# Optimization experiments

Measured on AMD Instinct MI355X. Metric: run time of the kernel, lower is better.

The kernel has to match this reference:

```python
import jax, jax.numpy as jnp
import numpy as np

L, D, H, R = 8, 1024, 16, 16
HD = D // H  # head dim


def setup_inputs() -> dict:
    key = jax.random.key(0)
    ks = jax.random.split(key, 7)
    s = 0.02  # init scale for stability
    return {
        "x": jax.random.normal(ks[0], (2, 1024, D), jnp.float32),
        "Wqkv": jax.random.normal(ks[1], (L, D, 3 * D), jnp.float32) * s,
        "Aqkv": jax.random.normal(ks[2], (L, D, R), jnp.float32) * s,
        "Bqkv": jax.random.normal(ks[3], (L, R, 3 * D), jnp.float32) * s,
        "Wproj": jax.random.normal(ks[4], (L, D, D), jnp.float32) * s,
        "Aproj": jax.random.normal(ks[5], (L, D, R), jnp.float32) * s,
        "Bproj": jax.random.normal(ks[6], (L, R, D), jnp.float32) * s,
    }


def _forward(x, Wqkv, Aqkv, Bqkv, Wproj, Aproj, Bproj):
    B, S, _ = x.shape
    # causal mask [S, S]
    mask = jnp.tril(jnp.ones((S, S), bool))

    def layer(h, p):
        Wq, Aq, Bq, Wp, Ap, Bp = p
        # LoRA merge exactly as the module: p + A @ B, then dense matmul
        Wq_m = Wq + Aq @ Bq            # [D, 3D]
        Wp_m = Wp + Ap @ Bp            # [D, D]
        qkv = h @ Wq_m                 # [B, S, 3D]
        q, k, v = jnp.split(qkv, 3, axis=-1)
        q = q.reshape(B, S, H, HD).transpose(0, 2, 1, 3)  # [B,H,S,hd]
        k = k.reshape(B, S, H, HD).transpose(0, 2, 1, 3)
        v = v.reshape(B, S, H, HD).transpose(0, 2, 1, 3)
        scores = jnp.einsum("bhqd,bhkd->bhqk", q, k) / np.sqrt(HD)
        scores = jnp.where(mask, scores, jnp.finfo(scores.dtype).min)
        attn = jax.nn.softmax(scores, axis=-1)
        o = jnp.einsum("bhqk,bhkd->bhqd", attn, v)        # [B,H,S,hd]
        o = o.transpose(0, 2, 1, 3).reshape(B, S, D)
        return h + o @ Wp_m, None

    out, _ = jax.lax.scan(layer, x, (Wqkv, Aqkv, Bqkv, Wproj, Aproj, Bproj))
    return out


def reference(x, Wqkv, Aqkv, Bqkv, Wproj, Aproj, Bproj):
    return _forward(x, Wqkv, Aqkv, Bqkv, Wproj, Aproj, Bproj)
```

## Files before the change

### kernel.cpp

```cpp
#include <hip/hip_runtime.h>
#include <hip/hip_bf16.h>


typedef unsigned short ushort_t;
typedef __attribute__((ext_vector_type(8))) short bf16x8;
typedef __attribute__((ext_vector_type(4))) float f32x4;

__device__ __forceinline__ unsigned short f2bf(float f) {
    union { float f; unsigned int u; } x; x.f = f;
    unsigned int r = x.u + 0x7fffu + ((x.u >> 16) & 1u);
    return (unsigned short)(r >> 16);
}

__device__ __forceinline__ f32x4 mfma16(bf16x8 a, bf16x8 b, f32x4 c) {
    return __builtin_amdgcn_mfma_f32_16x16x32_bf16(a, b, c, 0, 0, 0);
}

typedef const __attribute__((address_space(1))) unsigned int* gas_ptr;
typedef __attribute__((address_space(3))) unsigned int* las_ptr;
__device__ __forceinline__ void lds_stage16(const void* g, void* l) {
    __builtin_amdgcn_global_load_lds((gas_ptr)(unsigned long long)g,
                                     (las_ptr)(unsigned int)(unsigned long long)l,
                                     16, 0, 0);
}

#define RORMAX(x, C)                                                           \
    x = fmaxf(x, __int_as_float(__builtin_amdgcn_mov_dpp(                      \
                     __float_as_int(x), C, 0xf, 0xf, false)));
#define RORADD(x, C)                                                           \
    x += __int_as_float(__builtin_amdgcn_mov_dpp(                              \
        __float_as_int(x), C, 0xf, 0xf, false));

__global__ __launch_bounds__(256) void convert_x(
    const float4* __restrict__ in, float4* __restrict__ outF,
    ushort4* __restrict__ outB, int n4) {
    int i = blockIdx.x * 256 + threadIdx.x;
    if (i < n4) {
        float4 v = in[i];
        outF[i] = v;
        ushort4 o;
        o.x = f2bf(v.x); o.y = f2bf(v.y); o.z = f2bf(v.z); o.w = f2bf(v.w);
        outB[i] = o;
    }
}

__global__ __launch_bounds__(256) void merge_T2(
    const float* __restrict__ Wq, const float* __restrict__ Aq,
    const float* __restrict__ Bq, unsigned short* __restrict__ WTq,
    const float* __restrict__ Wp, const float* __restrict__ Ap,
    const float* __restrict__ Bp, unsigned short* __restrict__ WTp) {
    __shared__ float t[32][132];
    __shared__ float Asl[32][17];
    int bid = blockIdx.x;
    const float *W, *A, *Bm;
    unsigned short* WT;
    int N, bx, by, bz;
    if (bid < 6144) {
        N = 3072; bx = bid % 24; int u = bid / 24; by = u & 31; bz = u >> 5;
        W = Wq; A = Aq; Bm = Bq; WT = WTq;
    } else {
        bid -= 6144;
        N = 1024; bx = bid & 7; int u = bid >> 3; by = u & 31; bz = u >> 5;
        W = Wp; A = Ap; Bm = Bp; WT = WTp;
    }
    W  += (size_t)bz * 1024 * N;
    A  += (size_t)bz * 1024 * 16;
    Bm += (size_t)bz * 16 * N;
    WT += (size_t)bz * N * 1024;
    int j0 = bx * 128, i0 = by * 32;
    int tx = threadIdx.x & 31, ty = threadIdx.x >> 5;

    if (threadIdx.x < 128) {
        int r = threadIdx.x >> 2, c4 = (threadIdx.x & 3) * 4;
        float4 a = *(const float4*)&A[(size_t)(i0 + r) * 16 + c4];
        Asl[r][c4 + 0] = a.x; Asl[r][c4 + 1] = a.y;
        Asl[r][c4 + 2] = a.z; Asl[r][c4 + 3] = a.w;
    }
    float4 bv[16];
    #pragma unroll
    for (int r = 0; r < 16; r++)
        bv[r] = *(const float4*)&Bm[(size_t)r * N + j0 + tx * 4];
    float4 wv[4];
    #pragma unroll
    for (int ii0 = 0; ii0 < 4; ii0++)
        wv[ii0] = *(const float4*)&W[(size_t)(i0 + ty + ii0 * 8) * N + j0 + tx * 4];
    __builtin_amdgcn_sched_barrier(0);
    __syncthreads();

    #pragma unroll
    for (int ii0 = 0; ii0 < 4; ii0++) {
        int ii = ty + ii0 * 8;
        float4 acc = wv[ii0];
        #pragma unroll
        for (int r = 0; r < 16; r++) {
            float a = Asl[ii][r];
            acc.x += a * bv[r].x; acc.y += a * bv[r].y;
            acc.z += a * bv[r].z; acc.w += a * bv[r].w;
        }
        *(float4*)&t[ii][tx * 4] = acc;
    }
    __syncthreads();
    int jj = threadIdx.x >> 1, half = threadIdx.x & 1;
    bf16x8 o0, o1;
    #pragma unroll
    for (int c = 0; c < 8; c++) o0[c] = (short)f2bf(t[half * 16 + c][jj]);
    #pragma unroll
    for (int c = 0; c < 8; c++) o1[c] = (short)f2bf(t[half * 16 + 8 + c][jj]);
    unsigned short* dst = &WT[(size_t)(j0 + jj) * 1024 + i0 + half * 16];
    *(bf16x8*)dst = o0;
    *(bf16x8*)(dst + 8) = o1;
}

__global__ __launch_bounds__(256) void gemm_bf16_128(
    const unsigned short* __restrict__ A,
    const unsigned short* __restrict__ BT,
    unsigned short* __restrict__ outB,
    unsigned short* __restrict__ VT,
    int M, int N, int K) {
    __shared__ __align__(16) unsigned short As[2][128 * 32];
    __shared__ __align__(16) unsigned short Bs[2][128 * 32];
    const int tid = threadIdx.x;
    const int m0 = blockIdx.y * 128, n0 = blockIdx.x * 128;
    const int w = tid >> 6, lane = tid & 63;
    const int wm = (w >> 1) * 64, wn = (w & 1) * 64;
    const int lr = lane & 15, quad = lane >> 4;
    const int srow = w * 16 + (lane >> 2);
    const int skof = (lane & 3) * 8;

    f32x4 acc[4][4] = {};

    for (int k0 = 0; k0 < K; k0 += 64) {
        __syncthreads();
        #pragma unroll
        for (int h = 0; h < 2; h++) {
            lds_stage16(A  + (size_t)(m0 + srow)      * K + k0 + h * 32 + skof,
                        (char*)As[h] + w * 1024);
            lds_stage16(A  + (size_t)(m0 + 64 + srow) * K + k0 + h * 32 + skof,
                        (char*)As[h] + 4096 + w * 1024);
            lds_stage16(BT + (size_t)(n0 + srow)      * K + k0 + h * 32 + skof,
                        (char*)Bs[h] + w * 1024);
            lds_stage16(BT + (size_t)(n0 + 64 + srow) * K + k0 + h * 32 + skof,
                        (char*)Bs[h] + 4096 + w * 1024);
        }
        __syncthreads();

        #pragma unroll
        for (int h = 0; h < 2; h++) {
            bf16x8 af[4], bfr[4];
            #pragma unroll
            for (int i = 0; i < 4; i++) {
                af[i]  = *(const bf16x8*)&As[h][(wm + i * 16 + lr) * 32 + quad * 8];
                bfr[i] = *(const bf16x8*)&Bs[h][(wn + i * 16 + lr) * 32 + quad * 8];
            }
            #pragma unroll
            for (int i = 0; i < 4; i++)
                #pragma unroll
                for (int j = 0; j < 4; j++)
                    acc[i][j] = mfma16(af[i], bfr[j], acc[i][j]);
        }
    }
    if (n0 < 2048) {
        #pragma unroll
        for (int i = 0; i < 4; i++)
            #pragma unroll
            for (int j = 0; j < 4; j++)
                #pragma unroll
                for (int r = 0; r < 4; r++) {
                    int row = m0 + wm + i * 16 + quad * 4 + r;
                    int col = n0 + wn + j * 16 + lr;
                    float v = acc[i][j][r];
                    if (col < 1024) v *= 0.125f;
                    outB[(size_t)row * N + col] = f2bf(v);
                }
    } else {
        const int b = m0 >> 10;
        #pragma unroll
        for (int i = 0; i < 4; i++) {
            int row0 = m0 + wm + i * 16 + quad * 4;
            int s = row0 & 1023;
            #pragma unroll
            for (int j = 0; j < 4; j++) {
                int hd = n0 - 2048 + wn + j * 16 + lr;
                ushort4 o;
                o.x = f2bf(acc[i][j][0]); o.y = f2bf(acc[i][j][1]);
                o.z = f2bf(acc[i][j][2]); o.w = f2bf(acc[i][j][3]);
                *(ushort4*)&VT[((size_t)b * 1024 + hd) * 1024 + s] = o;
            }
        }
    }
}

__global__ __launch_bounds__(256) void gemm_bf16_64(
    const unsigned short* __restrict__ A,
    const unsigned short* __restrict__ BT,
    const float* __restrict__ res,
    float* __restrict__ outF,
    unsigned short* __restrict__ outB,
    int M, int N, int K) {
    __shared__ __align__(16) unsigned short As[2][2][64 * 32];
    __shared__ __align__(16) unsigned short Bs[2][2][64 * 32];
    const int tid = threadIdx.x;
    const int m0 = blockIdx.y * 64, n0 = blockIdx.x * 64;
    const int w = tid >> 6, lane = tid & 63;
    const int wm = (w >> 1) * 32, wn = (w & 1) * 32;
    const int lr = lane & 15, quad = lane >> 4;
    const int srow = w * 16 + (lane >> 2);
    const int skof = (lane & 3) * 8;

    f32x4 acc[2][2] = {};

    auto stage = [&](int k0, int buf) {
        #pragma unroll
        for (int h = 0; h < 2; h++) {
            lds_stage16(A  + (size_t)(m0 + srow) * K + k0 + h * 32 + skof,
                        (char*)As[buf][h] + w * 1024);
            lds_stage16(BT + (size_t)(n0 + srow) * K + k0 + h * 32 + skof,
                        (char*)Bs[buf][h] + w * 1024);
        }
    };

    const int nk = K >> 6;
    stage(0, 0);
    for (int t = 0; t < nk; t++) {
        __syncthreads();
        if (t + 1 < nk) stage((t + 1) << 6, (t + 1) & 1);
        const int cur = t & 1;
        #pragma unroll
        for (int h = 0; h < 2; h++) {
            bf16x8 af[2], bfr[2];
            #pragma unroll
            for (int i = 0; i < 2; i++) {
                af[i]  = *(const bf16x8*)&As[cur][h][(wm + i * 16 + lr) * 32 + quad * 8];
                bfr[i] = *(const bf16x8*)&Bs[cur][h][(wn + i * 16 + lr) * 32 + quad * 8];
            }
            #pragma unroll
            for (int i = 0; i < 2; i++)
                #pragma unroll
                for (int j = 0; j < 2; j++)
                    acc[i][j] = mfma16(af[i], bfr[j], acc[i][j]);
        }
    }
    #pragma unroll
    for (int i = 0; i < 2; i++)
        #pragma unroll
        for (int j = 0; j < 2; j++)
            #pragma unroll
            for (int r = 0; r < 4; r++) {
                int row = m0 + wm + i * 16 + quad * 4 + r;
                int col = n0 + wn + j * 16 + lr;
                float v = acc[i][j][r] + res[(size_t)row * N + col];
                if (outF) outF[(size_t)row * N + col] = v;
                if (outB) outB[(size_t)row * N + col] = f2bf(v);
            }
}

__global__ __launch_bounds__(256) void attn_kernel(
    const unsigned short* __restrict__ qkv,
    const unsigned short* __restrict__ VT,
    unsigned short* __restrict__ O) {
    __shared__ __align__(16) unsigned short Ks[2][2][64 * 32];
    __shared__ __align__(16) unsigned short Vs[2][2][64 * 32];
    __shared__ __align__(16) unsigned short pl[4][16 * 72];
    const int tid = threadIdx.x;
    const int w = tid >> 6, lane = tid & 63;
    const int lr = lane & 15, quad = lane >> 4;
    const int bh = blockIdx.y, b = bh >> 4, h = bh & 15;
    const int qblk = (bh < 16) ? blockIdx.x : (15 - blockIdx.x);
    const int qb = qblk * 64 + w * 16;
    const int srow = w * 16 + (lane >> 2);
    const int skof = (lane & 3) * 8;
    const float LOG2E = 1.44269504f;

    const size_t rowQ = (size_t)(b * 1024 + qb + lr) * 3072 + h * 64;
    bf16x8 aq0 = *(const bf16x8*)&qkv[rowQ + quad * 8];
    bf16x8 aq1 = *(const bf16x8*)&qkv[rowQ + 32 + quad * 8];

    float m_i[4], l_i[4];
    f32x4 oacc[4] = {};
    #pragma unroll
    for (int r = 0; r < 4; r++) { m_i[r] = -1e30f; l_i[r] = 0.f; }

    auto stage = [&](int kt64, int buf) {
        const int kt = kt64 << 6;
        const size_t gK = (size_t)(b * 1024 + kt + srow) * 3072 + 1024 + h * 64;
        lds_stage16(qkv + gK + skof,      (char*)Ks[buf][0] + w * 1024);
        lds_stage16(qkv + gK + 32 + skof, (char*)Ks[buf][1] + w * 1024);
        const size_t gV = ((size_t)bh * 64 + srow) * 1024 + kt;
        lds_stage16(VT + gV + skof,       (char*)Vs[buf][0] + w * 1024);
        lds_stage16(VT + gV + 32 + skof,  (char*)Vs[buf][1] + w * 1024);
    };

    const int nkt = qblk + 1;
    stage(0, 0);
    for (int kt64 = 0; kt64 < nkt; kt64++) {
        __syncthreads();
        if (kt64 + 1 < nkt) stage(kt64 + 1, (kt64 + 1) & 1);
        const int cur = kt64 & 1;
        const int kt = kt64 << 6;

        f32x4 s[4] = {};
        #pragma unroll
        for (int nh = 0; nh < 4; nh++) {
            bf16x8 kb0 = *(const bf16x8*)&Ks[cur][0][(nh * 16 + lr) * 32 + quad * 8];
            bf16x8 kb1 = *(const bf16x8*)&Ks[cur][1][(nh * 16 + lr) * 32 + quad * 8];
            s[nh] = mfma16(aq0, kb0, s[nh]);
            s[nh] = mfma16(aq1, kb1, s[nh]);
        }
        float mx[4];
        if (kt + 64 > qb) {
            #pragma unroll
            for (int r = 0; r < 4; r++) {
                int qrow = qb + quad * 4 + r;
                #pragma unroll
                for (int nh = 0; nh < 4; nh++) {
                    int kcol = kt + nh * 16 + lr;
                    s[nh][r] = (kcol <= qrow) ? s[nh][r] : -1e30f;
                }
            }
        }
        #pragma unroll
        for (int r = 0; r < 4; r++) {
            mx[r] = fmaxf(fmaxf(s[0][r], s[1][r]), fmaxf(s[2][r], s[3][r]));
            RORMAX(mx[r], 0x121) RORMAX(mx[r], 0x122)
            RORMAX(mx[r], 0x124) RORMAX(mx[r], 0x128)
        }
        float al[4];
        #pragma unroll
        for (int r = 0; r < 4; r++) {
            float mnew = fmaxf(m_i[r], mx[r]);
            al[r] = exp2f((m_i[r] - mnew) * LOG2E);
            m_i[r] = mnew;
            float lsum = 0.f;
            #pragma unroll
            for (int nh = 0; nh < 4; nh++) {
                float p = exp2f((s[nh][r] - mnew) * LOG2E);
                s[nh][r] = p;
                lsum += p;
            }
            l_i[r] = l_i[r] * al[r] + lsum;
        }
        #pragma unroll
        for (int dt = 0; dt < 4; dt++)
            #pragma unroll
            for (int r = 0; r < 4; r++) oacc[dt][r] *= al[r];
        #pragma unroll
        for (int nh = 0; nh < 4; nh++)
            #pragma unroll
            for (int r = 0; r < 4; r++)
                pl[w][(quad * 4 + r) * 72 + nh * 16 + lr] = f2bf(s[nh][r]);
        bf16x8 ap0 = *(const bf16x8*)&pl[w][lr * 72 + quad * 8];
        bf16x8 ap1 = *(const bf16x8*)&pl[w][lr * 72 + 32 + quad * 8];
        #pragma unroll
        for (int dt = 0; dt < 4; dt++) {
            bf16x8 vb0 = *(const bf16x8*)&Vs[cur][0][(dt * 16 + lr) * 32 + quad * 8];
            bf16x8 vb1 = *(const bf16x8*)&Vs[cur][1][(dt * 16 + lr) * 32 + quad * 8];
            oacc[dt] = mfma16(ap0, vb0, oacc[dt]);
            oacc[dt] = mfma16(ap1, vb1, oacc[dt]);
        }
    }
    #pragma unroll
    for (int r = 0; r < 4; r++) {
        RORADD(l_i[r], 0x121) RORADD(l_i[r], 0x122)
        RORADD(l_i[r], 0x124) RORADD(l_i[r], 0x128)
    }
    #pragma unroll
    for (int dt = 0; dt < 4; dt++)
        #pragma unroll
        for (int r = 0; r < 4; r++) {
            int row = b * 1024 + qb + quad * 4 + r;
            int col = h * 64 + dt * 16 + lr;
            O[(size_t)row * 1024 + col] = f2bf(oacc[dt][r] / l_i[r]);
        }
}

extern "C" void kernel_launch(void* const* d_in, const int* in_sizes, int n_in,
                              void* d_out, int out_size, void* d_ws, size_t ws_size,
                              hipStream_t stream) {
    const float* x     = (const float*)d_in[0];
    const float* Wqkv  = (const float*)d_in[1];
    const float* Aqkv  = (const float*)d_in[2];
    const float* Bqkv  = (const float*)d_in[3];
    const float* Wproj = (const float*)d_in[4];
    const float* Aproj = (const float*)d_in[5];
    const float* Bproj = (const float*)d_in[6];
    float* out = (float*)d_out;

    char* ws = (char*)d_ws;
    float* h_f32 = (float*)ws;                    ws += (size_t)2048 * 1024 * 4;
    unsigned short* h_bf   = (unsigned short*)ws; ws += (size_t)2048 * 1024 * 2;
    unsigned short* qkv_bf = (unsigned short*)ws; ws += (size_t)2048 * 3072 * 2;
    unsigned short* VT     = (unsigned short*)ws; ws += (size_t)32 * 64 * 1024 * 2;
    unsigned short* O_bf   = (unsigned short*)ws; ws += (size_t)2048 * 1024 * 2;
    unsigned short* WqT8   = (unsigned short*)ws; ws += (size_t)8 * 3072 * 1024 * 2;
    unsigned short* WpT8   = (unsigned short*)ws; ws += (size_t)8 * 1024 * 1024 * 2;

    convert_x<<<2048, 256, 0, stream>>>((const float4*)x, (float4*)h_f32,
                                        (ushort4*)h_bf, 2048 * 1024 / 4);
    merge_T2<<<8192, 256, 0, stream>>>(Wqkv, Aqkv, Bqkv, WqT8,
                                       Wproj, Aproj, Bproj, WpT8);

    for (int l = 0; l < 8; l++) {
        const unsigned short* WqT = WqT8 + (size_t)l * 3072 * 1024;
        const unsigned short* WpT = WpT8 + (size_t)l * 1024 * 1024;
        gemm_bf16_128<<<dim3(24, 16), 256, 0, stream>>>(h_bf, WqT, qkv_bf, VT,
                                                        2048, 3072, 1024);
        attn_kernel<<<dim3(16, 32), 256, 0, stream>>>(qkv_bf, VT, O_bf);
        float* outF = (l == 7) ? out : h_f32;
        gemm_bf16_64<<<dim3(16, 32), 256, 0, stream>>>(O_bf, WpT, h_f32, outF,
                                                       h_bf, 2048, 1024, 1024);
    }
}
```

Baseline: 717.0 us.

## Restructure LoRA merge to stage W via LDS and fold log2e into Q scale

The merge kernel now loads the W tile straight into LDS with asynchronous global-to-LDS copies. Each thread computes the A@B correction for its own output column while reading rows transposed from LDS, which removes one barrier and the intermediate transpose buffer. Separately, the log2(e) factor moves into the Q scaling in the QKV GEMM epilogue, so the attention softmax skips one multiply per exponential. The cost is more redundant Asl reads and scalar B loads per thread, plus Q rounded to bf16 after the extra scaling.

```diff
diff --git a/kernel.cpp b/kernel.cpp
--- a/kernel.cpp
+++ b/kernel.cpp
@@ -49,8 +49,8 @@
     const float* __restrict__ Bq, unsigned short* __restrict__ WTq,
     const float* __restrict__ Wp, const float* __restrict__ Ap,
     const float* __restrict__ Bp, unsigned short* __restrict__ WTp) {
-    __shared__ float t[32][132];
     __shared__ float Asl[32][17];
+    __shared__ __align__(16) float tW[32 * 128];
     int bid = blockIdx.x;
     const float *W, *A, *Bm;
     unsigned short* WT;
@@ -67,45 +67,42 @@
     A  += (size_t)bz * 1024 * 16;
     Bm += (size_t)bz * 16 * N;
     WT += (size_t)bz * N * 1024;
-    int j0 = bx * 128, i0 = by * 32;
-    int tx = threadIdx.x & 31, ty = threadIdx.x >> 5;
-
-    if (threadIdx.x < 128) {
-        int r = threadIdx.x >> 2, c4 = (threadIdx.x & 3) * 4;
+    const int j0 = bx * 128, i0 = by * 32;
+    const int tid = threadIdx.x;
+    const int w = tid >> 6, lane = tid & 63;
+
+    #pragma unroll
+    for (int s = 0; s < 4; s++) {
+        int w4s = w * 4 + s;
+        int tr = w4s * 2 + (lane >> 5);
+        lds_stage16(W + (size_t)(i0 + tr) * N + j0 + (lane & 31) * 4,
+                    (char*)tW + w4s * 1024);
+    }
+    if (tid < 128) {
+        int r = tid >> 2, c4 = (tid & 3) * 4;
         float4 a = *(const float4*)&A[(size_t)(i0 + r) * 16 + c4];
         Asl[r][c4 + 0] = a.x; Asl[r][c4 + 1] = a.y;
         Asl[r][c4 + 2] = a.z; Asl[r][c4 + 3] = a.w;
     }
-    float4 bv[16];
+    const int jj = tid >> 1, half = tid & 1;
+    float bcol[16];
     #pragma unroll
     for (int r = 0; r < 16; r++)
-        bv[r] = *(const float4*)&Bm[(size_t)r * N + j0 + tx * 4];
-    float4 wv[4];
-    #pragma unroll
-    for (int ii0 = 0; ii0 < 4; ii0++)
-        wv[ii0] = *(const float4*)&W[(size_t)(i0 + ty + ii0 * 8) * N + j0 + tx * 4];
+        bcol[r] = Bm[(size_t)r * N + j0 + jj];
     __builtin_amdgcn_sched_barrier(0);
     __syncthreads();
 
-    #pragma unroll
-    for (int ii0 = 0; ii0 < 4; ii0++) {
-        int ii = ty + ii0 * 8;
-        float4 acc = wv[ii0];
-        #pragma unroll
-        for (int r = 0; r < 16; r++) {
-            float a = Asl[ii][r];
-            acc.x += a * bv[r].x; acc.y += a * bv[r].y;
-            acc.z += a * bv[r].z; acc.w += a * bv[r].w;
-        }
-        *(float4*)&t[ii][tx * 4] = acc;
-    }
-    __syncthreads();
-    int jj = threadIdx.x >> 1, half = threadIdx.x & 1;
     bf16x8 o0, o1;
     #pragma unroll
-    for (int c = 0; c < 8; c++) o0[c] = (short)f2bf(t[half * 16 + c][jj]);
-    #pragma unroll
-    for (int c = 0; c < 8; c++) o1[c] = (short)f2bf(t[half * 16 + 8 + c][jj]);
+    for (int c = 0; c < 16; c++) {
+        int rloc = half * 16 + c;
+        float v = tW[rloc * 128 + jj];
+        #pragma unroll
+        for (int r = 0; r < 16; r++)
+            v += Asl[rloc][r] * bcol[r];
+        unsigned short b = f2bf(v);
+        if (c < 8) o0[c] = (short)b; else o1[c - 8] = (short)b;
+    }
     unsigned short* dst = &WT[(size_t)(j0 + jj) * 1024 + i0 + half * 16];
     *(bf16x8*)dst = o0;
     *(bf16x8*)(dst + 8) = o1;
@@ -169,7 +166,7 @@
                     int row = m0 + wm + i * 16 + quad * 4 + r;
                     int col = n0 + wn + j * 16 + lr;
                     float v = acc[i][j][r];
-                    if (col < 1024) v *= 0.125f;
+                    if (col < 1024) v *= 0.125f * 1.44269504f;
                     outB[(size_t)row * N + col] = f2bf(v);
                 }
     } else {
@@ -269,7 +266,6 @@
     const int qb = qblk * 64 + w * 16;
     const int srow = w * 16 + (lane >> 2);
     const int skof = (lane & 3) * 8;
-    const float LOG2E = 1.44269504f;
 
     const size_t rowQ = (size_t)(b * 1024 + qb + lr) * 3072 + h * 64;
     bf16x8 aq0 = *(const bf16x8*)&qkv[rowQ + quad * 8];
@@ -328,12 +324,12 @@
         #pragma unroll
         for (int r = 0; r < 4; r++) {
             float mnew = fmaxf(m_i[r], mx[r]);
-            al[r] = exp2f((m_i[r] - mnew) * LOG2E);
+            al[r] = exp2f(m_i[r] - mnew);
             m_i[r] = mnew;
             float lsum = 0.f;
             #pragma unroll
             for (int nh = 0; nh < 4; nh++) {
-                float p = exp2f((s[nh][r] - mnew) * LOG2E);
+                float p = exp2f(s[nh][r] - mnew);
                 s[nh][r] = p;
                 lsum += p;
             }
```

After: 710.0 us. No clear change (-1.0%).
